# Optimization experiments

Measured on AMD Instinct MI355X. Metric: run time of the kernel, lower is better.

The kernel has to match this reference:

```python
import jax, jax.numpy as jnp
import numpy as np

N_NODES = 100000
N_EDGES = 600000
N_GRAPHS = 256
D_IN, D_HID, N_CLS = 256, 128, 10
LEAKY_SLOPE = 0.01  # torch default


def gcn_conv(x, W, b, row, col, edge_weight, num_nodes):
    # PyG gcn_norm with add_self_loops=False:
    # deg[j] = sum of edge_weight into target j; norm = d^-1/2[row] * w * d^-1/2[col]
    deg = jax.ops.segment_sum(edge_weight, col, num_segments=num_nodes)
    dis = jnp.where(deg > 0, jax.lax.rsqrt(jnp.where(deg > 0, deg, 1.0)), 0.0)
    norm = dis[row] * edge_weight * dis[col]
    h = x @ W                                   # [N, H] dense GEMM first (as GCNConv does)
    msg = norm[:, None] * h[row]                # [E, H] gather + scale
    out = jax.ops.segment_sum(msg, col, num_segments=num_nodes)  # scatter-add
    return out + b


def setup_inputs() -> dict:
    key = jax.random.key(0)
    ks = jax.random.split(key, 10)
    x = jax.random.normal(ks[0], (N_NODES, D_IN), dtype=jnp.float32)
    edge_index = jax.random.randint(ks[1], (2, N_EDGES), 0, N_NODES, dtype=jnp.int64)
    edge_weight = jax.random.uniform(ks[2], (N_EDGES,), dtype=jnp.float32)
    batch = jnp.sort(jax.random.randint(ks[3], (N_NODES,), 0, N_GRAPHS, dtype=jnp.int64))
    s1 = 1.0 / np.sqrt(D_IN)
    s2 = 1.0 / np.sqrt(D_HID)
    W1 = jax.random.uniform(ks[4], (D_IN, D_HID), jnp.float32, -s1, s1)
    b1 = jnp.zeros((D_HID,), jnp.float32)
    W2 = jax.random.uniform(ks[5], (D_HID, D_HID), jnp.float32, -s2, s2)
    b2 = jnp.zeros((D_HID,), jnp.float32)
    Wl = jax.random.uniform(ks[6], (D_HID, N_CLS), jnp.float32, -s2, s2)
    bl = jax.random.uniform(ks[7], (N_CLS,), jnp.float32, -s2, s2)
    return {"x": x, "edge_index": edge_index, "edge_weight": edge_weight, "batch": batch,
            "W1": W1, "b1": b1, "W2": W2, "b2": b2, "Wl": Wl, "bl": bl}


def reference(x, edge_index, edge_weight, batch, W1, b1, W2, b2, Wl, bl):
    # Eval-mode forward: dropout is identity (training=False).
    row, col = edge_index[0], edge_index[1]
    h = gcn_conv(x, W1, b1, row, col, edge_weight, N_NODES)
    h = jnp.where(h >= 0, h, LEAKY_SLOPE * h)
    h = gcn_conv(h, W2, b2, row, col, edge_weight, N_NODES)
    h = jnp.where(h >= 0, h, LEAKY_SLOPE * h)
    # global mean pool over graphs
    sums = jax.ops.segment_sum(h, batch, num_segments=N_GRAPHS)          # [G, H]
    cnts = jax.ops.segment_sum(jnp.ones((h.shape[0],), h.dtype), batch, num_segments=N_GRAPHS)
    pooled = sums / jnp.maximum(cnts, 1.0)[:, None]
    logits = pooled @ Wl + bl
    return jax.nn.log_softmax(logits, axis=1)
```

## Files before the change

### kernel.cpp

```cpp
#include <hip/hip_runtime.h>

typedef float f32x4 __attribute__((ext_vector_type(4)));
typedef short bf16x8 __attribute__((ext_vector_type(8)));

#define SLOPE 0.01f
#define BKT 64

__device__ __forceinline__ short f2bf(float f) {
    unsigned int u = __float_as_uint(f);
    unsigned int r = (u + 0x7fffu + ((u >> 16) & 1u)) >> 16;
    return (short)r;
}

__global__ void k_init(const float* __restrict__ W1, const float* __restrict__ W2,
                       short* __restrict__ wf1, short* __restrict__ wf2,
                       int* __restrict__ cnt,
                       float* __restrict__ sums, float* __restrict__ cnts, int N, int G) {
    int t = blockIdx.x * blockDim.x + threadIdx.x;
    if (t < 4096) {
        int ntile = t >> 9;
        int ks = (t >> 6) & 7;
        int lane = t & 63;
        int h = lane >> 4, c = lane & 15;
#pragma unroll
        for (int j = 0; j < 8; j++) {
            int k = ks * 32 + h * 8 + j;
            wf1[t * 8 + j] = f2bf(W1[k * 128 + ntile * 16 + c]);
        }
    } else if (t < 6144) {
        int s = t - 4096;
        int ntile = s >> 8;
        int ks = (s >> 6) & 3;
        int lane = s & 63;
        int h = lane >> 4, c = lane & 15;
#pragma unroll
        for (int j = 0; j < 8; j++) {
            int k = ks * 32 + h * 8 + j;
            wf2[s * 8 + j] = f2bf(W2[k * 128 + ntile * 16 + c]);
        }
    } else {
        long u = t - 6144;
        if (u < N) cnt[u] = 0;
        else {
            long v = u - N;
            if (v < (long)G * 128) sums[v] = 0.f;
            else if (v < (long)G * 128 + G) cnts[v - (long)G * 128] = 0.f;
        }
    }
}

__global__ __launch_bounds__(256, 3) void k_gemm1_hist(
        const float* __restrict__ Av, const short* __restrict__ Wf,
        ushort* __restrict__ out, int M, int gemmBlocks,
        const int* __restrict__ ei, const float* __restrict__ ew,
        int* __restrict__ cnt, uint2* __restrict__ ebuf,
        int E, int histBlocks) {
    __shared__ short lds[4 * 8 * 64 * 8];
    const int tid = threadIdx.x;
    int b = blockIdx.x;
    int nInter = 2 * (gemmBlocks < histBlocks ? gemmBlocks : histBlocks);
    bool isGemm; int idx;
    if (b < nInter) { isGemm = (b & 1) == 0; idx = b >> 1; }
    else {
        int r = b - nInter;
        if (gemmBlocks < histBlocks) { isGemm = false; idx = gemmBlocks + r; }
        else                         { isGemm = true;  idx = histBlocks + r; }
    }

    if (!isGemm) {
        int i = idx * 256 + tid;
        int stride = histBlocks * 256;
#pragma unroll
        for (int k = 0; k < 4; k++, i += stride)
            if (i < E) {
                int c = ei[E + i];
                int pos = atomicAdd(&cnt[c], 1);
                if (pos < BKT)
                    ebuf[(long)c * BKT + pos] = make_uint2((unsigned)ei[i], __float_as_uint(ew[i]));
            }
        return;
    }

    const int lane = tid & 63;
    const int wid = tid >> 6;
    const int h = lane >> 4, c = lane & 15;
    const int rowW = idx * 128 + wid * 32;

    bf16x8 afr[2][8];
#pragma unroll
    for (int rg = 0; rg < 2; rg++) {
        int arow = rowW + rg * 16 + c;
        if (arow >= M) arow = M - 1;
        const float* arp = Av + (long)arow * 256 + h * 8;
#pragma unroll
        for (int ks = 0; ks < 8; ks++) {
            float4 a0 = *(const float4*)(arp + ks * 32);
            float4 a1 = *(const float4*)(arp + ks * 32 + 4);
            bf16x8 f;
            f[0] = f2bf(a0.x); f[1] = f2bf(a0.y); f[2] = f2bf(a0.z); f[3] = f2bf(a0.w);
            f[4] = f2bf(a1.x); f[5] = f2bf(a1.y); f[6] = f2bf(a1.z); f[7] = f2bf(a1.w);
            afr[rg][ks] = f;
        }
    }

    const bf16x8* lf8 = (const bf16x8*)lds;
#pragma unroll
    for (int half = 0; half < 2; half++) {
        if (half) __syncthreads();
        {
            const float4* wsrc = (const float4*)Wf + half * 2048;
            float4* wdst = (float4*)lds;
#pragma unroll
            for (int i = 0; i < 8; i++)
                wdst[i * 256 + tid] = wsrc[i * 256 + tid];
        }
        __syncthreads();
#pragma unroll
        for (int ntl = 0; ntl < 4; ntl++) {
            int nt = half * 4 + ntl;
            bf16x8 bfr[8];
#pragma unroll
            for (int ks = 0; ks < 8; ks++)
                bfr[ks] = lf8[(ntl * 8 + ks) * 64 + lane];
            f32x4 acc0 = {0.f, 0.f, 0.f, 0.f}, acc1 = {0.f, 0.f, 0.f, 0.f};
#pragma unroll
            for (int ks = 0; ks < 8; ks++) {
                acc0 = __builtin_amdgcn_mfma_f32_16x16x32_bf16(bfr[ks], afr[0][ks], acc0, 0, 0, 0);
                acc1 = __builtin_amdgcn_mfma_f32_16x16x32_bf16(bfr[ks], afr[1][ks], acc1, 0, 0, 0);
            }
#pragma unroll
            for (int rg = 0; rg < 2; rg++) {
                f32x4 acc = rg ? acc1 : acc0;
                int orow = rowW + rg * 16 + c;
                if (orow < M) {
                    ushort4 pk;
                    pk.x = (ushort)f2bf(acc[0]); pk.y = (ushort)f2bf(acc[1]);
                    pk.z = (ushort)f2bf(acc[2]); pk.w = (ushort)f2bf(acc[3]);
                    *(ushort4*)(out + (long)orow * 128 + nt * 16 + h * 4) = pk;
                }
            }
        }
    }
}

__global__ void k_degdis(const int* __restrict__ cnt, const uint2* __restrict__ ebuf,
                         float* __restrict__ dis, int N) {
    int n = blockIdx.x * blockDim.x + threadIdx.x;
    if (n >= N) return;
    int m = cnt[n];
    const uint2* p = ebuf + (long)n * BKT;
    float d = 0.f;
    for (int i = 0; i < m; i++) d += __uint_as_float(p[i].y);
    dis[n] = d > 0.f ? rsqrtf(d) : 0.f;
}

__global__ __launch_bounds__(256, 4) void k_gemm2(const ushort* __restrict__ Av,
                                                  const short* __restrict__ Wf,
                                                  ushort* __restrict__ out, int M) {
    __shared__ short lds[4 * 8 * 64 * 8];
    const int tid = threadIdx.x;
    {
        const float4* wsrc = (const float4*)Wf;
        float4* wdst = (float4*)lds;
#pragma unroll
        for (int i = 0; i < 8; i++)
            wdst[i * 256 + tid] = wsrc[i * 256 + tid];
    }
    __syncthreads();

    const int lane = tid & 63;
    const int wid = tid >> 6;
    const int h = lane >> 4, c = lane & 15;
    const int rowW = blockIdx.x * 128 + wid * 32;

    bf16x8 afr[2][4];
#pragma unroll
    for (int rg = 0; rg < 2; rg++) {
        int arow = rowW + rg * 16 + c;
        if (arow >= M) arow = M - 1;
        const ushort* arp = Av + (long)arow * 128 + h * 8;
#pragma unroll
        for (int ks = 0; ks < 4; ks++)
            afr[rg][ks] = *(const bf16x8*)(arp + ks * 32);
    }

    const bf16x8* lf8 = (const bf16x8*)lds;
#pragma unroll
    for (int nt = 0; nt < 8; nt++) {
        bf16x8 bfr[4];
#pragma unroll
        for (int ks = 0; ks < 4; ks++)
            bfr[ks] = lf8[(nt * 4 + ks) * 64 + lane];
        f32x4 acc0 = {0.f, 0.f, 0.f, 0.f}, acc1 = {0.f, 0.f, 0.f, 0.f};
#pragma unroll
        for (int ks = 0; ks < 4; ks++) {
            acc0 = __builtin_amdgcn_mfma_f32_16x16x32_bf16(bfr[ks], afr[0][ks], acc0, 0, 0, 0);
            acc1 = __builtin_amdgcn_mfma_f32_16x16x32_bf16(bfr[ks], afr[1][ks], acc1, 0, 0, 0);
        }
#pragma unroll
        for (int rg = 0; rg < 2; rg++) {
            f32x4 acc = rg ? acc1 : acc0;
            int orow = rowW + rg * 16 + c;
            if (orow < M) {
                ushort4 pk;
                pk.x = (ushort)f2bf(acc[0]); pk.y = (ushort)f2bf(acc[1]);
                pk.z = (ushort)f2bf(acc[2]); pk.w = (ushort)f2bf(acc[3]);
                *(ushort4*)(out + (long)orow * 128 + nt * 16 + h * 4) = pk;
            }
        }
    }
}

template <int OM>
__global__ __launch_bounds__(256) void k_agg(const uint2* __restrict__ ebuf,
                                             const int* __restrict__ cnt, const float* __restrict__ dis,
                                             const unsigned* __restrict__ hbuf,
                                             unsigned* __restrict__ outp, const float* __restrict__ bias, int N) {
    int wv = (blockIdx.x * blockDim.x + threadIdx.x) >> 6;
    int lane = threadIdx.x & 63;
    if (wv >= N) return;
    long s = (long)wv * BKT;
    int m = cnt[wv];
    float discol = dis[wv];
    float ax = 0.f, ay = 0.f;
    for (int base = 0; base < m; base += 16) {
        int rem = m - base;
        int nact = rem < 16 ? rem : 16;
        uint2 p = make_uint2(0u, 0u);
        float dr = 0.f;
        if (lane < nact) { p = ebuf[s + base + lane]; dr = dis[p.x]; }
        float nrmL = dr * __uint_as_float(p.y) * discol;
        int px = (int)p.x;
#pragma unroll
        for (int j = 0; j < 8; j++) {
            unsigned rj = (unsigned)__shfl(px, j);
            float nj = __shfl(nrmL, j);
            unsigned hv = hbuf[(long)rj * 64 + lane];
            ax = fmaf(nj, __uint_as_float(hv << 16), ax);
            ay = fmaf(nj, __uint_as_float(hv & 0xffff0000u), ay);
        }
        if (rem > 8) {
#pragma unroll
            for (int j = 8; j < 16; j++) {
                unsigned rj = (unsigned)__shfl(px, j);
                float nj = __shfl(nrmL, j);
                unsigned hv = hbuf[(long)rj * 64 + lane];
                ax = fmaf(nj, __uint_as_float(hv << 16), ax);
                ay = fmaf(nj, __uint_as_float(hv & 0xffff0000u), ay);
            }
        }
    }
    float vx = ax, vy = ay;
    if (OM == 0) {
        float2 bv = ((const float2*)bias)[lane];
        vx += bv.x; vx = vx < 0.f ? SLOPE * vx : vx;
        vy += bv.y; vy = vy < 0.f ? SLOPE * vy : vy;
    }
    unsigned pk = (unsigned)(ushort)f2bf(vx) | ((unsigned)(ushort)f2bf(vy) << 16);
    outp[(long)wv * 64 + lane] = pk;
}

__global__ __launch_bounds__(64) void k_pool(const unsigned* __restrict__ aggb, const float* __restrict__ b2,
                                             const int* __restrict__ batch, float* __restrict__ sums,
                                             float* __restrict__ cnts, int N) {
    int n0 = blockIdx.x * 128;
    if (n0 >= N) return;
    int t = threadIdx.x;
    float2 bv = ((const float2*)b2)[t];
    int end = min(n0 + 128, N);
    int curg = batch[n0];
    float ax = 0.f, ay = 0.f;
    int run = 0;
    for (int n = n0; n < end; n++) {
        int g = batch[n];
        if (g != curg) {
            atomicAdd(&sums[curg * 128 + 2 * t], ax);
            atomicAdd(&sums[curg * 128 + 2 * t + 1], ay);
            if (t == 0) atomicAdd(&cnts[curg], (float)run);
            ax = ay = 0.f; run = 0; curg = g;
        }
        unsigned pk = aggb[(long)n * 64 + t];
        float vx = __uint_as_float(pk << 16) + bv.x;        vx = vx < 0.f ? SLOPE * vx : vx;
        float vy = __uint_as_float(pk & 0xffff0000u) + bv.y; vy = vy < 0.f ? SLOPE * vy : vy;
        ax += vx; ay += vy; run++;
    }
    atomicAdd(&sums[curg * 128 + 2 * t], ax);
    atomicAdd(&sums[curg * 128 + 2 * t + 1], ay);
    if (t == 0) atomicAdd(&cnts[curg], (float)run);
}

__global__ void k_final(const float* __restrict__ sums, const float* __restrict__ cnts,
                        const float* __restrict__ Wl, const float* __restrict__ bl,
                        float* __restrict__ out, int G) {
    int g = blockIdx.x * blockDim.x + threadIdx.x;
    if (g >= G) return;
    float inv = 1.f / fmaxf(cnts[g], 1.f);
    float l[10];
#pragma unroll
    for (int c = 0; c < 10; c++) l[c] = bl[c];
    for (int k = 0; k < 128; k++) {
        float p = sums[g * 128 + k] * inv;
#pragma unroll
        for (int c = 0; c < 10; c++) l[c] += p * Wl[k * 10 + c];
    }
    float m = l[0];
#pragma unroll
    for (int c = 1; c < 10; c++) m = fmaxf(m, l[c]);
    float s = 0.f;
#pragma unroll
    for (int c = 0; c < 10; c++) s += expf(l[c] - m);
    float lse = m + logf(s);
#pragma unroll
    for (int c = 0; c < 10; c++) out[g * 10 + c] = l[c] - lse;
}

extern "C" void kernel_launch(void* const* d_in, const int* in_sizes, int n_in,
                              void* d_out, int out_size, void* d_ws, size_t ws_size,
                              hipStream_t stream) {
    const float* x  = (const float*)d_in[0];
    const int*   ei = (const int*)d_in[1];
    const float* ew = (const float*)d_in[2];
    const int*   batch = (const int*)d_in[3];
    const float* W1 = (const float*)d_in[4];
    const float* b1 = (const float*)d_in[5];
    const float* W2 = (const float*)d_in[6];
    const float* b2 = (const float*)d_in[7];
    const float* Wl = (const float*)d_in[8];
    const float* bl = (const float*)d_in[9];
    float* out = (float*)d_out;

    const int N = in_sizes[0] / 256;
    const int E = in_sizes[2];
    const int G = out_size / 10;

    char* ws = (char*)d_ws;
    float*  dis  = (float*)(ws);
    int*    cnt  = (int*)  (ws + 400384);
    uint2*  ebuf = (uint2*)(ws + 800768);
    ushort* hbuf = (ushort*)(ws + 52000768);
    ushort* abuf = (ushort*)(ws + 77600768);
    short*  wf1  = (short*)(ws + 103200768);
    short*  wf2  = (short*)(ws + 103266304);
    float*  sums = (float*)(ws + 103299072);
    float*  cnts = (float*)(ws + 103430144);

    long initThreads = 6144 + (long)N + (long)G * 128 + G;
    int initBlocks = (int)((initThreads + 255) / 256);
    k_init<<<initBlocks, 256, 0, stream>>>(W1, W2, wf1, wf2, cnt, sums, cnts, N, G);

    const int GB = (N + 127) / 128;
    const int HB = (E + 1023) / 1024;
    k_gemm1_hist<<<GB + HB, 256, 0, stream>>>(x, wf1, hbuf, N, GB,
                                              ei, ew, cnt, ebuf, E, HB);

    k_degdis<<<(N + 255) / 256, 256, 0, stream>>>(cnt, ebuf, dis, N);

    k_agg<0><<<(N + 3) / 4, 256, 0, stream>>>(ebuf, cnt, dis, (const unsigned*)hbuf, (unsigned*)abuf, b1, N);
    k_gemm2<<<(N + 127) / 128, 256, 0, stream>>>(abuf, wf2, hbuf, N);
    k_agg<1><<<(N + 3) / 4, 256, 0, stream>>>(ebuf, cnt, dis, (const unsigned*)hbuf, (unsigned*)abuf, nullptr, N);

    k_pool<<<(N + 127) / 128, 64, 0, stream>>>((const unsigned*)abuf, b2, batch, sums, cnts, N);
    k_final<<<1, 256, 0, stream>>>(sums, cnts, Wl, bl, out, G);
}
```

Before: 199.4 us.

## Precompute edge norms once, parallelize degree sum, batch histogram loads

```diff
diff --git a/kernel.cpp b/kernel.cpp
--- a/kernel.cpp
+++ b/kernel.cpp
@@ -68,16 +68,21 @@
     }
 
     if (!isGemm) {
-        int i = idx * 256 + tid;
+        int base = idx * 256 + tid;
         int stride = histBlocks * 256;
-#pragma unroll
-        for (int k = 0; k < 4; k++, i += stride)
-            if (i < E) {
-                int c = ei[E + i];
-                int pos = atomicAdd(&cnt[c], 1);
-                if (pos < BKT)
-                    ebuf[(long)c * BKT + pos] = make_uint2((unsigned)ei[i], __float_as_uint(ew[i]));
-            }
+        int iv[4]; bool av[4]; int cv[4]; int rv[4]; float wv2[4]; int pv[4];
+#pragma unroll
+        for (int k = 0; k < 4; k++) { iv[k] = base + k * stride; av[k] = iv[k] < E; }
+#pragma unroll
+        for (int k = 0; k < 4; k++) if (av[k]) cv[k] = ei[E + iv[k]];
+#pragma unroll
+        for (int k = 0; k < 4; k++) if (av[k]) { rv[k] = ei[iv[k]]; wv2[k] = ew[iv[k]]; }
+#pragma unroll
+        for (int k = 0; k < 4; k++) if (av[k]) pv[k] = atomicAdd(&cnt[cv[k]], 1);
+#pragma unroll
+        for (int k = 0; k < 4; k++)
+            if (av[k] && pv[k] < BKT)
+                ebuf[(long)cv[k] * BKT + pv[k]] = make_uint2((unsigned)rv[k], __float_as_uint(wv2[k]));
         return;
     }
 
@@ -145,13 +150,32 @@
 
 __global__ void k_degdis(const int* __restrict__ cnt, const uint2* __restrict__ ebuf,
                          float* __restrict__ dis, int N) {
-    int n = blockIdx.x * blockDim.x + threadIdx.x;
+    int gid = blockIdx.x * blockDim.x + threadIdx.x;
+    int n = gid >> 3, e = gid & 7;
     if (n >= N) return;
     int m = cnt[n];
     const uint2* p = ebuf + (long)n * BKT;
     float d = 0.f;
-    for (int i = 0; i < m; i++) d += __uint_as_float(p[i].y);
-    dis[n] = d > 0.f ? rsqrtf(d) : 0.f;
+    for (int i = e; i < m; i += 8) d += __uint_as_float(p[i].y);
+    d += __shfl_xor(d, 1);
+    d += __shfl_xor(d, 2);
+    d += __shfl_xor(d, 4);
+    if (e == 0) dis[n] = d > 0.f ? rsqrtf(d) : 0.f;
+}
+
+__global__ void k_norm(const int* __restrict__ cnt, const float* __restrict__ dis,
+                       uint2* __restrict__ ebuf, int N) {
+    int gid = blockIdx.x * blockDim.x + threadIdx.x;
+    int n = gid >> 3, e = gid & 7;
+    if (n >= N) return;
+    int m = cnt[n];
+    float dc = dis[n];
+    uint2* p = ebuf + (long)n * BKT;
+    for (int i = e; i < m; i += 8) {
+        uint2 v = p[i];
+        float nr = dis[v.x] * __uint_as_float(v.y) * dc;
+        p[i].y = __float_as_uint(nr);
+    }
 }
 
 __global__ __launch_bounds__(256, 4) void k_gemm2(const ushort* __restrict__ Av,
@@ -213,7 +237,7 @@
 
 template <int OM>
 __global__ __launch_bounds__(256) void k_agg(const uint2* __restrict__ ebuf,
-                                             const int* __restrict__ cnt, const float* __restrict__ dis,
+                                             const int* __restrict__ cnt,
                                              const unsigned* __restrict__ hbuf,
                                              unsigned* __restrict__ outp, const float* __restrict__ bias, int N) {
     int wv = (blockIdx.x * blockDim.x + threadIdx.x) >> 6;
@@ -221,20 +245,17 @@
     if (wv >= N) return;
     long s = (long)wv * BKT;
     int m = cnt[wv];
-    float discol = dis[wv];
     float ax = 0.f, ay = 0.f;
     for (int base = 0; base < m; base += 16) {
         int rem = m - base;
         int nact = rem < 16 ? rem : 16;
         uint2 p = make_uint2(0u, 0u);
-        float dr = 0.f;
-        if (lane < nact) { p = ebuf[s + base + lane]; dr = dis[p.x]; }
-        float nrmL = dr * __uint_as_float(p.y) * discol;
-        int px = (int)p.x;
+        if (lane < nact) p = ebuf[s + base + lane];
+        int px = (int)p.x, py = (int)p.y;
 #pragma unroll
         for (int j = 0; j < 8; j++) {
             unsigned rj = (unsigned)__shfl(px, j);
-            float nj = __shfl(nrmL, j);
+            float nj = __uint_as_float((unsigned)__shfl(py, j));
             unsigned hv = hbuf[(long)rj * 64 + lane];
             ax = fmaf(nj, __uint_as_float(hv << 16), ax);
             ay = fmaf(nj, __uint_as_float(hv & 0xffff0000u), ay);
@@ -243,7 +264,7 @@
 #pragma unroll
             for (int j = 8; j < 16; j++) {
                 unsigned rj = (unsigned)__shfl(px, j);
-                float nj = __shfl(nrmL, j);
+                float nj = __uint_as_float((unsigned)__shfl(py, j));
                 unsigned hv = hbuf[(long)rj * 64 + lane];
                 ax = fmaf(nj, __uint_as_float(hv << 16), ax);
                 ay = fmaf(nj, __uint_as_float(hv & 0xffff0000u), ay);
@@ -353,11 +374,12 @@
     k_gemm1_hist<<<GB + HB, 256, 0, stream>>>(x, wf1, hbuf, N, GB,
                                               ei, ew, cnt, ebuf, E, HB);
 
-    k_degdis<<<(N + 255) / 256, 256, 0, stream>>>(cnt, ebuf, dis, N);
-
-    k_agg<0><<<(N + 3) / 4, 256, 0, stream>>>(ebuf, cnt, dis, (const unsigned*)hbuf, (unsigned*)abuf, b1, N);
+    k_degdis<<<(N * 8 + 255) / 256, 256, 0, stream>>>(cnt, ebuf, dis, N);
+    k_norm<<<(N * 8 + 255) / 256, 256, 0, stream>>>(cnt, dis, ebuf, N);
+
+    k_agg<0><<<(N + 3) / 4, 256, 0, stream>>>(ebuf, cnt, (const unsigned*)hbuf, (unsigned*)abuf, b1, N);
     k_gemm2<<<(N + 127) / 128, 256, 0, stream>>>(abuf, wf2, hbuf, N);
-    k_agg<1><<<(N + 3) / 4, 256, 0, stream>>>(ebuf, cnt, dis, (const unsigned*)hbuf, (unsigned*)abuf, nullptr, N);
+    k_agg<1><<<(N + 3) / 4, 256, 0, stream>>>(ebuf, cnt, (const unsigned*)hbuf, (unsigned*)abuf, nullptr, N);
 
     k_pool<<<(N + 127) / 128, 64, 0, stream>>>((const unsigned*)abuf, b2, batch, sums, cnts, N);
     k_final<<<1, 256, 0, stream>>>(sums, cnts, Wl, bl, out, G);
```

Result: no change. 195.6 us (-1.9%).
